# Kernel optimization log

Measured on AMD Instinct MI355X. Metric: run time of the kernel, lower is better.

Reference implementation:

```python
import jax, jax.numpy as jnp
import numpy as np

OBS_DIM, ACTION_DIM, H, FC = 64, 100, 512, 256
IN_DIM = FC + ACTION_DIM


def setup_inputs() -> dict:
    key = jax.random.key(0)
    ks = jax.random.split(key, 10)
    s = lambda k, shp, fan: jax.random.normal(k, shp, jnp.float32) * (1.0 / np.sqrt(fan))
    return {
        "observations": jax.random.normal(ks[0], (32, 2048, OBS_DIM), jnp.float32),
        "actions": jax.random.uniform(ks[1], (32, 2048), jnp.float32),
        "W_obs": s(ks[2], (OBS_DIM, FC), OBS_DIM), "b_obs": jnp.zeros((FC,), jnp.float32),
        "W_act": s(ks[3], (1, ACTION_DIM), 1), "b_act": jnp.zeros((ACTION_DIM,), jnp.float32),
        "W_lstm": s(ks[4], (IN_DIM, 4 * H), IN_DIM),
        "U_lstm": s(ks[5], (H, 4 * H), H),
        "b_lstm": jnp.zeros((4 * H,), jnp.float32),
        "W_proj": s(ks[6], (H, ACTION_DIM), H), "b_proj": jnp.zeros((ACTION_DIM,), jnp.float32),
    }


def _lstm_seq(x, W, U, b):
    # x: [B, T, D] -> outputs [B, T, H]; keras LSTMCell default activations.
    B = x.shape[0]
    h0 = jnp.zeros((B, H), x.dtype)
    c0 = jnp.zeros((B, H), x.dtype)

    def step(carry, x_t):
        h, c = carry
        z = x_t @ W + h @ U + b  # [B, 4H]
        i, f, g, o = jnp.split(z, 4, axis=-1)
        i = jax.nn.sigmoid(i); f = jax.nn.sigmoid(f)
        g = jnp.tanh(g); o = jax.nn.sigmoid(o)
        c = f * c + i * g
        h = o * jnp.tanh(c)
        return (h, c), h

    _, hs = jax.lax.scan(step, (h0, c0), jnp.swapaxes(x, 0, 1))  # [T, B, H]
    return jnp.swapaxes(hs, 0, 1)


def reference(observations, actions, W_obs, b_obs, W_act, b_act,
              W_lstm, U_lstm, b_lstm, W_proj, b_proj):
    a = jax.nn.relu(actions[..., None] @ W_act + b_act)        # [B, T, A]
    ob = jax.nn.relu(observations @ W_obs + b_obs)             # [B, T, FC]
    x = jnp.concatenate([ob, a], axis=-1)                      # [B, T, FC+A]
    seq = _lstm_seq(x, W_lstm, U_lstm, b_lstm)                 # [B, T, H]
    logits = seq @ W_proj + b_proj                             # [B, T, A]
    pi = jax.nn.softmax(logits, axis=-1)
    # tf.math.argmax(logits) defaults to axis=0 (over batch), kept faithfully.
    argmax_actions = jnp.argmax(logits, axis=0)
    return pi, logits, argmax_actions
```

## Files before the change

### kernel.cpp

```cpp
#include <hip/hip_runtime.h>
#include <cstdint>
#include <cstddef>

#define B_   32
#define T_   2048
#define OBS_ 64
#define FC_  256
#define ACT_ 100
#define H_   512
#define TC_  128
#define NCH_ 16

typedef __attribute__((ext_vector_type(4))) unsigned int u32x4;
typedef __attribute__((ext_vector_type(8))) short bf16x8;
typedef __attribute__((ext_vector_type(4))) float f32x4;

static __device__ __forceinline__ bf16x8 as_b(u32x4 v){ union{u32x4 u; bf16x8 b;} x; x.u=v; return x.b; }
static __device__ __forceinline__ unsigned short f2bf(float f){
  unsigned int u = __builtin_bit_cast(unsigned int, f);
  return (unsigned short)((u + 0x7fffu + ((u>>16)&1u)) >> 16);
}
static __device__ __forceinline__ float bf2f(unsigned short s){
  unsigned int u = ((unsigned int)s) << 16;
  return __builtin_bit_cast(float, u);
}
static __device__ __forceinline__ void split3(float v, unsigned short& h, unsigned short& m, unsigned short& l){
  h = f2bf(v);
  float r1 = v - bf2f(h);
  m = f2bf(r1);
  float r2 = r1 - bf2f(m);
  l = f2bf(r2);
}
static __device__ __forceinline__ u32x4 pack8(const unsigned short* v){
  u32x4 r;
  r.x = (unsigned)v[0] | ((unsigned)v[1]<<16);
  r.y = (unsigned)v[2] | ((unsigned)v[3]<<16);
  r.z = (unsigned)v[4] | ((unsigned)v[5]<<16);
  r.w = (unsigned)v[6] | ((unsigned)v[7]<<16);
  return r;
}
static __device__ __forceinline__ u32x4 load_cohx4(const unsigned int* p){
  u32x4 r;
  asm volatile("global_load_dwordx4 %0, %1, off sc0 sc1"
               : "=&v"(r) : "v"(p) : "memory");
  return r;
}

static constexpr size_t XF_OFF    = 0;
static constexpr size_t XF_SZ     = (size_t)TC_*2*12*3*64*16;
static constexpr size_t WF_OFF    = XF_OFF + XF_SZ;
static constexpr size_t WF_SZ     = (size_t)32*4*28*3*64*16;
static constexpr size_t WPF_OFF   = WF_OFF + WF_SZ;
static constexpr size_t WPF_SZ    = (size_t)7*16*3*64*16;
static constexpr size_t ZX_OFF    = WPF_OFF + WPF_SZ;
static constexpr size_t ZX_SZ     = (size_t)TC_*2*2048*16*4;
static constexpr size_t HC01_OFF  = ZX_OFF + ZX_SZ;
static constexpr size_t HC01_SZ   = (size_t)TC_*2*16*512*4;
static constexpr size_t HG_OFF    = HC01_OFF + HC01_SZ;
static constexpr size_t HG_SZ     = (size_t)3*2*16*2*256*4;
static constexpr size_t CST_OFF   = HG_OFF + HG_SZ;
static constexpr size_t CST_SZ    = (size_t)B_*H_*4;
static constexpr size_t CTR_OFF   = CST_OFF + CST_SZ;
static constexpr size_t CTR_SZ    = (size_t)2*T_*4;

__global__ __launch_bounds__(256) void k_prep_x(
    const float* __restrict__ obs, const float* __restrict__ act,
    const float* __restrict__ Wobs, const float* __restrict__ bobs,
    const float* __restrict__ Wact, const float* __restrict__ bact,
    u32x4* __restrict__ Xf, int tbase)
{
  __shared__ float Wl[64][257];
  __shared__ float ol[32][64];
  __shared__ float xr[32][256];
  __shared__ float al[32];
  __shared__ float wal[100], bal[100], bol[256];
  int tl = blockIdx.x; int t = tbase + tl; int tid = threadIdx.x;
  for (int i = tid; i < 64*256; i += 256) Wl[i>>8][i&255] = Wobs[i];
  for (int i = tid; i < 32*64; i += 256)
    ol[i>>6][i&63] = obs[((size_t)(i>>6)*T_ + t)*OBS_ + (i&63)];
  if (tid < 32) al[tid] = act[(size_t)tid*T_ + t];
  if (tid < 100) { wal[tid] = Wact[tid]; bal[tid] = bact[tid]; }
  bol[tid] = bobs[tid];
  __syncthreads();
  {
    int k = tid;
    double accd[32];
#pragma unroll
    for (int r = 0; r < 32; ++r) accd[r] = 0.0;
    for (int kc = 0; kc < 64; kc += 8) {
      float w[8];
#pragma unroll
      for (int q = 0; q < 8; ++q) w[q] = Wl[kc+q][k];
#pragma unroll
      for (int r = 0; r < 32; ++r) {
#pragma unroll
        for (int q = 0; q < 8; ++q) accd[r] += (double)w[q]*(double)ol[r][kc+q];
      }
    }
#pragma unroll
    for (int r = 0; r < 32; ++r) xr[r][k] = fmaxf((float)(accd[r] + (double)bol[k]), 0.f);
  }
  __syncthreads();
  int g = tid >> 6, l = tid & 63;
  int r = l & 15, sub = l >> 4;
  for (int p = g; p < 24; p += 4) {
    int bg = p / 12, kk = p % 12;
    int b = bg*16 + r;
    unsigned short vh[8], vm[8], vl[8];
#pragma unroll
    for (int j = 0; j < 8; ++j) {
      int k = kk*32 + sub*8 + j;
      float x;
      if (k < 256)      x = xr[b][k];
      else if (k < 356) {
        double tmp = (double)al[b]*(double)wal[k-256] + (double)bal[k-256];
        x = fmaxf((float)tmp, 0.f);
      } else            x = 0.f;
      split3(x, vh[j], vm[j], vl[j]);
    }
    size_t base = ((((size_t)tl*2 + bg)*12 + kk)*3)*64 + l;
    Xf[base]       = pack8(vh);
    Xf[base + 64]  = pack8(vm);
    Xf[base + 128] = pack8(vl);
  }
}

__global__ __launch_bounds__(256) void k_prep_w(
    const float* __restrict__ Wl, const float* __restrict__ Ul,
    unsigned short* __restrict__ Wf)
{
  size_t gid = (size_t)blockIdx.x*256 + threadIdx.x;
  if (gid >= (size_t)896*2048) return;
  int k = (int)(gid >> 11), oc = (int)(gid & 2047);
  float v = 0.f;
  if (k < 356) v = Wl[(size_t)k*2048 + oc];
  else if (k >= 384) v = Ul[(size_t)(k-384)*2048 + oc];
  unsigned short vh, vm, vlo;
  split3(v, vh, vm, vlo);
  int g = oc >> 9, hu = oc & 511;
  int hs = hu >> 4, wv = (hu >> 2) & 3, u = hu & 3;
  int cc = g*4 + u;
  int kk = k >> 5, sub = (k >> 3) & 3, j = k & 7;
  size_t e = ((((size_t)(hs*4 + wv)*28 + kk)*3 + 0)*64 + (sub*16 + cc))*8 + j;
  Wf[e]        = vh;
  Wf[e + 512]  = vm;
  Wf[e + 1024] = vlo;
}

__global__ __launch_bounds__(256) void k_prep_wp(
    const float* __restrict__ Wp, unsigned short* __restrict__ Wpf)
{
  int gid = blockIdx.x*256 + threadIdx.x;
  if (gid >= 512*112) return;
  int k = gid / 112, c = gid % 112;
  float v = (c < 100) ? Wp[(size_t)k*100 + c] : 0.f;
  unsigned short vh, vm, vlo;
  split3(v, vh, vm, vlo);
  int ct = c >> 4, cl = c & 15;
  int kk = k >> 5, sub = (k >> 3) & 3, j = k & 7;
  size_t e = (((size_t)(ct*16 + kk)*3 + 0)*64 + (sub*16 + cl))*8 + j;
  Wpf[e]        = vh;
  Wpf[e + 512]  = vm;
  Wpf[e + 1024] = vlo;
}

__global__ __launch_bounds__(256) void k_prep_zx(
    const u32x4* __restrict__ Xf, const u32x4* __restrict__ Wf,
    const float* __restrict__ blstm, float* __restrict__ zxT)
{
  int bid = blockIdx.x;
  int hq = bid & 7, bg = (bid >> 3) & 1, tl = bid >> 4;
  int tid = threadIdx.x;
  int v = tid >> 6, lane = tid & 63;
  int cc = lane & 15; int g = cc >> 2, u = cc & 3;
  int rbase = (lane >> 4) * 4;
  u32x4 xa[12][3];
  const u32x4* xp = Xf + (((size_t)tl*2 + bg)*12*3)*64 + lane;
#pragma unroll
  for (int f = 0; f < 12; ++f)
#pragma unroll
    for (int p = 0; p < 3; ++p) xa[f][p] = xp[(f*3+p)*64];
  for (int hi = 0; hi < 4; ++hi) {
    int hs = hq*4 + hi;
    const u32x4* bp = Wf + (((size_t)(hs*4 + v)*28)*3)*64 + lane;
    f32x4 a0={0,0,0,0},a1={0,0,0,0},a2={0,0,0,0},a3={0,0,0,0},a4={0,0,0,0},a5={0,0,0,0};
#pragma unroll
    for (int f = 0; f < 12; ++f) {
      u32x4 b0 = bp[(f*3+0)*64], b1 = bp[(f*3+1)*64], b2 = bp[(f*3+2)*64];
      a0 = __builtin_amdgcn_mfma_f32_16x16x32_bf16(as_b(xa[f][0]), as_b(b0), a0, 0,0,0);
      a1 = __builtin_amdgcn_mfma_f32_16x16x32_bf16(as_b(xa[f][0]), as_b(b1), a1, 0,0,0);
      a2 = __builtin_amdgcn_mfma_f32_16x16x32_bf16(as_b(xa[f][1]), as_b(b0), a2, 0,0,0);
      a3 = __builtin_amdgcn_mfma_f32_16x16x32_bf16(as_b(xa[f][0]), as_b(b2), a3, 0,0,0);
      a4 = __builtin_amdgcn_mfma_f32_16x16x32_bf16(as_b(xa[f][2]), as_b(b0), a4, 0,0,0);
      a5 = __builtin_amdgcn_mfma_f32_16x16x32_bf16(as_b(xa[f][1]), as_b(b1), a5, 0,0,0);
    }
    int oc = g*512 + hs*16 + v*4 + u;
    double bb = (double)blstm[oc];
    f32x4 st;
#pragma unroll
    for (int q = 0; q < 4; ++q) {
      double z = (((double)a3[q]+(double)a4[q])+(double)a5[q])
               + ((double)a1[q]+(double)a2[q]) + (double)a0[q] + bb;
      st[q] = (float)z;
    }
    *(f32x4*)(zxT + ((size_t)((size_t)(tl*2 + bg)*2048 + oc))*16 + rbase) = st;
  }
}

__global__ __launch_bounds__(256, 1) void k_rnn(
    const u32x4* __restrict__ Wf, const float* __restrict__ zxT,
    unsigned int* __restrict__ HC01,
    unsigned int* __restrict__ hg32, int* __restrict__ ctr,
    float* __restrict__ cstate, int tbase)
{
  int wg = blockIdx.x, bg = wg >> 5, hs = wg & 31;
  int tid = threadIdx.x, wv = tid >> 6, lane = tid & 63;
  int cc = lane & 15;
  int g = cc >> 2, u = cc & 3;
  int rbase = (lane >> 4) * 4;
  int U = hs*16 + wv*4 + u;
  const u32x4* bp = Wf + ((((size_t)(hs*4 + wv)*28) + 12)*3)*64 + lane;
  float c[4];
#pragma unroll
  for (int q = 0; q < 4; ++q)
    c[q] = cstate[(size_t)(bg*16 + rbase + q)*512 + U];
  int Ue = hs*16 + wv*4 + (u & 2);
  int wkk = Ue >> 5, wsub = (Ue >> 3) & 3, wwrd = (Ue >> 1) & 3;

  u32x4 wa[16], wb[16];
#pragma unroll
  for (int kk = 0; kk < 16; ++kk) { wa[kk] = bp[(kk*3+0)*64]; wb[kk] = bp[(kk*3+1)*64]; }
  f32x4 zx = *(const f32x4*)(zxT + ((size_t)((size_t)(0*2 + bg)*2048 + g*512 + U))*16 + rbase);

#pragma unroll 1
  for (int tl = 0; tl < TC_; ++tl) {
    int gt = tbase + tl;
    if (tl > 0) {
      if (tid == 0) {
        const int* cp = ctr + ((size_t)bg*T_ + (gt-1));
        int cv;
        for (;;) {
          asm volatile("global_load_dword %0, %1, off sc0 sc1\n\t"
                       "s_waitcnt vmcnt(0)"
                       : "=&v"(cv) : "v"(cp) : "memory");
          if (cv >= 32) break;
          __builtin_amdgcn_s_sleep(1);
        }
      }
      __syncthreads();
    }
    u32x4 hf0[16], hf1[16];
    {
      const unsigned int* hbase = hg32 + ((size_t)((gt+2)%3)*2 + bg)*16*2*256 + lane*4;
#pragma unroll
      for (int kk = 0; kk < 16; ++kk) {
        hf0[kk] = load_cohx4(hbase + (kk*2+0)*256);
        hf1[kk] = load_cohx4(hbase + (kk*2+1)*256);
      }
    }
    asm volatile("s_waitcnt vmcnt(0)" ::: "memory");
    __builtin_amdgcn_sched_barrier(0);
    f32x4 a0={0,0,0,0},a1={0,0,0,0},a2={0,0,0,0};
#pragma unroll
    for (int kk = 0; kk < 16; ++kk) {
      a0 = __builtin_amdgcn_mfma_f32_16x16x32_bf16(as_b(hf0[kk]), as_b(wa[kk]), a0, 0,0,0);
      a1 = __builtin_amdgcn_mfma_f32_16x16x32_bf16(as_b(hf0[kk]), as_b(wb[kk]), a1, 0,0,0);
      a2 = __builtin_amdgcn_mfma_f32_16x16x32_bf16(as_b(hf1[kk]), as_b(wa[kk]), a2, 0,0,0);
    }
    float hv[4];
#pragma unroll
    for (int q = 0; q < 4; ++q) {
      float z = (a1[q] + a2[q]) + a0[q] + zx[q];
      float o0 = __shfl_xor(z, 4, 64);
      float e0 = (g & 1) ? o0 : z;
      float e1 = (g & 1) ? z  : o0;
      float p0 = __shfl_xor(e0, 8, 64);
      float p1 = __shfl_xor(e1, 8, 64);
      float zi = (g & 2) ? p0 : e0;
      float zf = (g & 2) ? p1 : e1;
      float zg = (g & 2) ? e0 : p0;
      float zo = (g & 2) ? e1 : p1;
      float i_ = 1.f/(1.f + expf(-zi));
      float f_ = 1.f/(1.f + expf(-zf));
      float g_ = tanhf(zg);
      float o_ = 1.f/(1.f + expf(-zo));
      c[q] = f_*c[q] + i_*g_;
      hv[q] = o_*tanhf(c[q]);
    }
    unsigned int* ringW = hg32 + ((size_t)(gt%3)*2 + bg)*16*2*256;
#pragma unroll
    for (int q = 0; q < 4; ++q) {
      float hq = hv[q];
      float hp = __shfl_xor(hq, 1, 64);
      unsigned short h0o = f2bf(hq);
      unsigned short h1o = f2bf(hq - bf2f(h0o));
      if (g == 0) {
        size_t hcidx = ((size_t)(tl*2 + bg)*16 + rbase + q)*512 + U;
        HC01[hcidx] = (unsigned)h0o | ((unsigned)h1o << 16);
        if (!(u & 1)) {
          unsigned short h0p = f2bf(hp);
          unsigned short h1p = f2bf(hp - bf2f(h0p));
          unsigned int w0 = (unsigned)h0o | ((unsigned)h0p << 16);
          unsigned int w1 = (unsigned)h1o | ((unsigned)h1p << 16);
          size_t d0 = ((size_t)wkk*2 + 0)*256 + (wsub*16 + rbase + q)*4 + wwrd;
          __hip_atomic_store(&ringW[d0],       w0, __ATOMIC_RELAXED, __HIP_MEMORY_SCOPE_AGENT);
          __hip_atomic_store(&ringW[d0 + 256], w1, __ATOMIC_RELAXED, __HIP_MEMORY_SCOPE_AGENT);
        }
      }
    }
    if (tl < TC_-1) {
      __syncthreads();
      if (tid == 0)
        __hip_atomic_fetch_add(&ctr[(size_t)bg*T_ + gt], 1, __ATOMIC_RELAXED, __HIP_MEMORY_SCOPE_AGENT);
      zx = *(const f32x4*)(zxT + ((size_t)((size_t)((tl+1)*2 + bg)*2048 + g*512 + U))*16 + rbase);
#pragma unroll
      for (int kk = 0; kk < 16; ++kk) { wa[kk] = bp[(kk*3+0)*64]; wb[kk] = bp[(kk*3+1)*64]; }
    }
  }
#pragma unroll
  for (int q = 0; q < 4; ++q)
    if (g == 0) cstate[(size_t)(bg*16 + rbase + q)*512 + U] = c[q];
}

__global__ __launch_bounds__(256) void k_logits(
    const unsigned int* __restrict__ HC01,
    const u32x4* __restrict__ Wpf,
    const float* __restrict__ bproj, float* __restrict__ out, int tbase)
{
  __shared__ float zl[16][120];
  int bid = blockIdx.x;
  int tl = bid >> 1, bg = bid & 1;
  int tid = threadIdx.x;
  int w = tid >> 6, lane = tid & 63;
  int row = lane & 15, koff = (lane >> 4) * 8;
  u32x4 a[16][2];
  {
    const unsigned int* h01 = HC01 + (((size_t)tl*2 + bg)*16 + row)*512 + koff;
#pragma unroll
    for (int kk = 0; kk < 16; ++kk) {
      u32x4 c0 = *(const u32x4*)(h01 + 32*kk);
      u32x4 c1 = *(const u32x4*)(h01 + 32*kk + 4);
      u32x4 p0, p1;
      p0.x = (c0.x & 0xffffu) | (c0.y << 16);
      p0.y = (c0.z & 0xffffu) | (c0.w << 16);
      p0.z = (c1.x & 0xffffu) | (c1.y << 16);
      p0.w = (c1.z & 0xffffu) | (c1.w << 16);
      p1.x = (c0.x >> 16) | (c0.y & 0xffff0000u);
      p1.y = (c0.z >> 16) | (c0.w & 0xffff0000u);
      p1.z = (c1.x >> 16) | (c1.y & 0xffff0000u);
      p1.w = (c1.z >> 16) | (c1.w & 0xffff0000u);
      a[kk][0] = p0;
      a[kk][1] = p1;
    }
  }
  for (int ct = w; ct < 7; ct += 4) {
    f32x4 c0 = {0,0,0,0}, c1 = {0,0,0,0}, c2 = {0,0,0,0};
    const u32x4* bp2 = Wpf + ((size_t)ct*16*3)*64 + lane;
#pragma unroll
    for (int kk = 0; kk < 16; ++kk) {
      u32x4 b0 = bp2[(kk*3+0)*64], b1 = bp2[(kk*3+1)*64];
      c0 = __builtin_amdgcn_mfma_f32_16x16x32_bf16(as_b(a[kk][0]), as_b(b0), c0, 0,0,0);
      c1 = __builtin_amdgcn_mfma_f32_16x16x32_bf16(as_b(a[kk][0]), as_b(b1), c1, 0,0,0);
      c2 = __builtin_amdgcn_mfma_f32_16x16x32_bf16(as_b(a[kk][1]), as_b(b0), c2, 0,0,0);
    }
    int col = ct*16 + (lane & 15);
    float bv = (col < 100) ? bproj[col] : 0.f;
#pragma unroll
    for (int q = 0; q < 4; ++q) {
      double z = ((double)c1[q] + (double)c2[q]) + (double)c0[q] + (double)bv;
      if (col < 120) zl[(lane>>4)*4 + q][col] = (float)z;
    }
  }
  __syncthreads();
  int srow = tid >> 4, l16 = tid & 15;
  float vv[7];
  float m = -1e30f;
#pragma unroll
  for (int k2 = 0; k2 < 7; ++k2) {
    int col = l16 + 16*k2;
    vv[k2] = (col < 100) ? zl[srow][col] : -1e30f;
    m = fmaxf(m, vv[k2]);
  }
#pragma unroll
  for (int d = 1; d < 16; d <<= 1) m = fmaxf(m, __shfl_xor(m, d, 64));
  float s = 0.f; float ek[7];
#pragma unroll
  for (int k2 = 0; k2 < 7; ++k2) {
    int col = l16 + 16*k2;
    ek[k2] = (col < 100) ? expf(vv[k2] - m) : 0.f;
    s += ek[k2];
  }
#pragma unroll
  for (int d = 1; d < 16; d <<= 1) s += __shfl_xor(s, d, 64);
  int t = tbase + tl; int b = bg*16 + srow;
  float* piout = out;
  float* lgout = out + 6553600ull;
#pragma unroll
  for (int k2 = 0; k2 < 7; ++k2) {
    int col = l16 + 16*k2;
    if (col < 100) {
      size_t idx = ((size_t)b*T_ + t)*100 + col;
      lgout[idx] = vv[k2];
      piout[idx] = ek[k2] / s;
    }
  }
}

__global__ __launch_bounds__(128) void k_argmax(
    const float* __restrict__ lg, float* __restrict__ outA)
{
  int t = blockIdx.x, j = threadIdx.x;
  if (j >= 100) return;
  float best = lg[(size_t)t*100 + j];
  int bi = 0;
  for (int b = 1; b < 32; ++b) {
    float v = lg[((size_t)b*T_ + t)*100 + j];
    if (v > best) { best = v; bi = b; }
  }
  outA[(size_t)t*100 + j] = (float)bi;
}

extern "C" void kernel_launch(void* const* d_in, const int* in_sizes, int n_in,
                              void* d_out, int out_size, void* d_ws, size_t ws_size,
                              hipStream_t stream) {
  const float* obs  = (const float*)d_in[0];
  const float* act  = (const float*)d_in[1];
  const float* Wobs = (const float*)d_in[2];
  const float* bobs = (const float*)d_in[3];
  const float* Wact = (const float*)d_in[4];
  const float* bact = (const float*)d_in[5];
  const float* Wl   = (const float*)d_in[6];
  const float* Ul   = (const float*)d_in[7];
  const float* bl   = (const float*)d_in[8];
  const float* Wp   = (const float*)d_in[9];
  const float* bp   = (const float*)d_in[10];
  char* ws = (char*)d_ws;
  u32x4* Xf             = (u32x4*)(ws + XF_OFF);
  unsigned short* WfS   = (unsigned short*)(ws + WF_OFF);
  unsigned short* WpfS  = (unsigned short*)(ws + WPF_OFF);
  float* zxT            = (float*)(ws + ZX_OFF);
  unsigned int* HC01    = (unsigned int*)(ws + HC01_OFF);
  unsigned int* hg32    = (unsigned int*)(ws + HG_OFF);
  float* cstate         = (float*)(ws + CST_OFF);
  int* ctr              = (int*)(ws + CTR_OFF);
  float* out = (float*)d_out;

  hipMemsetAsync(ws + HG_OFF, 0, HG_SZ + CST_SZ + CTR_SZ, stream);
  k_prep_w<<<7168, 256, 0, stream>>>(Wl, Ul, WfS);
  k_prep_wp<<<(512*112 + 255)/256, 256, 0, stream>>>(Wp, WpfS);
  for (int ch = 0; ch < NCH_; ++ch) {
    int tb = ch * TC_;
    k_prep_x<<<TC_, 256, 0, stream>>>(obs, act, Wobs, bobs, Wact, bact, Xf, tb);
    k_prep_zx<<<TC_*2*8, 256, 0, stream>>>((const u32x4*)Xf, (const u32x4*)WfS, bl, zxT);
    k_rnn<<<64, 256, 0, stream>>>((const u32x4*)WfS, zxT, HC01,
                                  hg32, ctr, cstate, tb);
    k_logits<<<TC_*2, 256, 0, stream>>>(HC01, (const u32x4*)WpfS, bp, out, tb);
  }
  k_argmax<<<T_, 128, 0, stream>>>(out + 6553600ull, out + 13107200ull);
}
```

Before: 12.50 ms.

## Shard step counters across cache lines and stage hidden state via LDS

Splits each per-timestep arrival counter into four counters on separate 64-byte-strided slots, so atomic increments from different workgroups contend less, and the poller sums the four. Each workgroup now loads the shared hidden-state vector cooperatively once into LDS with contiguous coherent loads per thread. Each wave then reads its MFMA operands from LDS instead of every wave issuing its own 32 coherent global loads. This adds an extra __syncthreads, LDS traffic and a larger counter buffer, and the poll issues four loads per iteration.

```diff
diff --git a/kernel.cpp b/kernel.cpp
--- a/kernel.cpp
+++ b/kernel.cpp
@@ -61,7 +61,7 @@
 static constexpr size_t CST_OFF   = HG_OFF + HG_SZ;
 static constexpr size_t CST_SZ    = (size_t)B_*H_*4;
 static constexpr size_t CTR_OFF   = CST_OFF + CST_SZ;
-static constexpr size_t CTR_SZ    = (size_t)2*T_*4;
+static constexpr size_t CTR_SZ    = (size_t)2*T_*64*4;
 
 __global__ __launch_bounds__(256) void k_prep_x(
     const float* __restrict__ obs, const float* __restrict__ act,
@@ -213,6 +213,7 @@
     unsigned int* __restrict__ hg32, int* __restrict__ ctr,
     float* __restrict__ cstate, int tbase)
 {
+  __shared__ u32x4 hst[2048];
   int wg = blockIdx.x, bg = wg >> 5, hs = wg & 31;
   int tid = threadIdx.x, wv = tid >> 6, lane = tid & 63;
   int cc = lane & 15;
@@ -237,35 +238,48 @@
     int gt = tbase + tl;
     if (tl > 0) {
       if (tid == 0) {
-        const int* cp = ctr + ((size_t)bg*T_ + (gt-1));
-        int cv;
+        const int* cb = ctr + ((size_t)bg*T_ + (gt-1))*64;
+        int v0, v1, v2, v3;
         for (;;) {
-          asm volatile("global_load_dword %0, %1, off sc0 sc1\n\t"
+          asm volatile("global_load_dword %0, %4, off sc0 sc1\n\t"
+                       "global_load_dword %1, %5, off sc0 sc1\n\t"
+                       "global_load_dword %2, %6, off sc0 sc1\n\t"
+                       "global_load_dword %3, %7, off sc0 sc1\n\t"
                        "s_waitcnt vmcnt(0)"
-                       : "=&v"(cv) : "v"(cp) : "memory");
-          if (cv >= 32) break;
+                       : "=&v"(v0), "=&v"(v1), "=&v"(v2), "=&v"(v3)
+                       : "v"(cb), "v"(cb+16), "v"(cb+32), "v"(cb+48) : "memory");
+          if (v0 + v1 + v2 + v3 >= 32) break;
           __builtin_amdgcn_s_sleep(1);
         }
       }
       __syncthreads();
     }
-    u32x4 hf0[16], hf1[16];
     {
-      const unsigned int* hbase = hg32 + ((size_t)((gt+2)%3)*2 + bg)*16*2*256 + lane*4;
-#pragma unroll
-      for (int kk = 0; kk < 16; ++kk) {
-        hf0[kk] = load_cohx4(hbase + (kk*2+0)*256);
-        hf1[kk] = load_cohx4(hbase + (kk*2+1)*256);
-      }
-    }
-    asm volatile("s_waitcnt vmcnt(0)" ::: "memory");
-    __builtin_amdgcn_sched_barrier(0);
+      const unsigned int* sbase = hg32 + ((size_t)((gt+2)%3)*2 + bg)*16*2*256 + tid*32;
+      u32x4 s0 = load_cohx4(sbase);
+      u32x4 s1 = load_cohx4(sbase + 4);
+      u32x4 s2 = load_cohx4(sbase + 8);
+      u32x4 s3 = load_cohx4(sbase + 12);
+      u32x4 s4 = load_cohx4(sbase + 16);
+      u32x4 s5 = load_cohx4(sbase + 20);
+      u32x4 s6 = load_cohx4(sbase + 24);
+      u32x4 s7 = load_cohx4(sbase + 28);
+      asm volatile("s_waitcnt vmcnt(0)" ::: "memory");
+      __builtin_amdgcn_sched_barrier(0);
+      hst[tid*8 + 0] = s0; hst[tid*8 + 1] = s1;
+      hst[tid*8 + 2] = s2; hst[tid*8 + 3] = s3;
+      hst[tid*8 + 4] = s4; hst[tid*8 + 5] = s5;
+      hst[tid*8 + 6] = s6; hst[tid*8 + 7] = s7;
+    }
+    __syncthreads();
     f32x4 a0={0,0,0,0},a1={0,0,0,0},a2={0,0,0,0};
 #pragma unroll
     for (int kk = 0; kk < 16; ++kk) {
-      a0 = __builtin_amdgcn_mfma_f32_16x16x32_bf16(as_b(hf0[kk]), as_b(wa[kk]), a0, 0,0,0);
-      a1 = __builtin_amdgcn_mfma_f32_16x16x32_bf16(as_b(hf0[kk]), as_b(wb[kk]), a1, 0,0,0);
-      a2 = __builtin_amdgcn_mfma_f32_16x16x32_bf16(as_b(hf1[kk]), as_b(wa[kk]), a2, 0,0,0);
+      u32x4 h0 = hst[(kk*2+0)*64 + lane];
+      u32x4 h1 = hst[(kk*2+1)*64 + lane];
+      a0 = __builtin_amdgcn_mfma_f32_16x16x32_bf16(as_b(h0), as_b(wa[kk]), a0, 0,0,0);
+      a1 = __builtin_amdgcn_mfma_f32_16x16x32_bf16(as_b(h0), as_b(wb[kk]), a1, 0,0,0);
+      a2 = __builtin_amdgcn_mfma_f32_16x16x32_bf16(as_b(h1), as_b(wa[kk]), a2, 0,0,0);
     }
     float hv[4];
 #pragma unroll
@@ -311,7 +325,8 @@
     if (tl < TC_-1) {
       __syncthreads();
       if (tid == 0)
-        __hip_atomic_fetch_add(&ctr[(size_t)bg*T_ + gt], 1, __ATOMIC_RELAXED, __HIP_MEMORY_SCOPE_AGENT);
+        __hip_atomic_fetch_add(ctr + ((size_t)bg*T_ + gt)*64 + (wg & 3)*16, 1,
+                               __ATOMIC_RELAXED, __HIP_MEMORY_SCOPE_AGENT);
       zx = *(const f32x4*)(zxT + ((size_t)((size_t)((tl+1)*2 + bg)*2048 + g*512 + U))*16 + rbase);
 #pragma unroll
       for (int kk = 0; kk < 16; ++kk) { wa[kk] = bp[(kk*3+0)*64]; wb[kk] = bp[(kk*3+1)*64]; }
```

Result: slower. 14.97 ms (+19.8%).
